# Optimization experiments

Measured on AMD Instinct MI355X. Metric: run time of the kernel, lower is better.

Reference implementation:

```python
import jax, jax.numpy as jnp
import numpy as np

D = 128

def _intra(nei, h, h_ref, att):
    # att: [2D] split into ref part and neighbor part; leakyrelu(cat(h_ref, nei_emb) @ att)
    a_ref, a_nei = att[:D], att[D:]
    nei_emb = h[nei]                                   # [N, S, D] gather
    s = h_ref @ a_ref                                  # [N]
    s = s[:, None] + nei_emb @ a_nei                   # [N, S]
    w = jax.nn.softmax(jax.nn.leaky_relu(s), axis=1)   # [N, S]
    return jnp.einsum('ns,nsd->nd', w, nei_emb)        # [N, D]

def _inter(embeds, fcW, fcb, att_inter):
    sps = jnp.stack([jnp.tanh(e @ fcW.T + fcb).mean(axis=0) for e in embeds])  # [T, D]
    beta = jax.nn.softmax(sps @ att_inter)             # [T]
    return sum(b * e for b, e in zip(beta, embeds))

def setup_inputs() -> dict:
    key = jax.random.key(0)
    ks = jax.random.split(key, 10)
    N, M, S1, S2 = 50000, 50000, 20, 10
    return {
        'h_ref': jax.random.normal(ks[0], (N, D), jnp.float32),
        'h1': jax.random.normal(ks[1], (M, D), jnp.float32),
        'h2': jax.random.normal(ks[2], (M, D), jnp.float32),
        'nei1': jax.random.randint(ks[3], (N, S1), 0, M),
        'nei2': jax.random.randint(ks[4], (N, S2), 0, M),
        'att1': jax.random.normal(ks[5], (2 * D,), jnp.float32) * 0.1,
        'att2': jax.random.normal(ks[6], (2 * D,), jnp.float32) * 0.1,
        'fcW': jax.random.normal(ks[7], (D, D), jnp.float32) * 0.1,
        'fcb': jnp.zeros((D,), jnp.float32),
        'att_inter': jax.random.normal(ks[8], (D,), jnp.float32) * 0.1,
    }

def reference(h_ref, h1, h2, nei1, nei2, att1, att2, fcW, fcb, att_inter):
    e1 = jax.nn.elu(_intra(nei1, h1, h_ref, att1))
    e2 = jax.nn.elu(_intra(nei2, h2, h_ref, att2))
    return _inter([e1, e2], fcW, fcb, att_inter)
```

## Files before the change

### kernel.cpp

```cpp
#include <hip/hip_runtime.h>
#include <hip/hip_bf16.h>
#include <math.h>

#define D 128
#define NB2 392
#define NWAVES (NB2 * 4)

typedef __attribute__((ext_vector_type(8))) short bf16x8;
typedef __attribute__((ext_vector_type(4))) float f32x4;

__device__ __forceinline__ float wave_sum(float v) {
#pragma unroll
  for (int off = 32; off; off >>= 1) v += __shfl_xor(v, off, 64);
  return v;
}

__device__ __forceinline__ unsigned bfr(float f) {
  const unsigned u = __float_as_uint(f);
  return (u + 0x7FFFu + ((u >> 16) & 1u)) >> 16;
}

__device__ __forceinline__ float fast_tanh(float x) {
  const float ez = __expf(2.f * x);
  return 1.f - 2.f / (ez + 1.f);
}

__global__ __launch_bounds__(256) void k_proj(
    const float* __restrict__ h_ref, const float* __restrict__ h1,
    const float* __restrict__ h2,
    const float* __restrict__ att1, const float* __restrict__ att2,
    float* __restrict__ q1, float* __restrict__ q2,
    float* __restrict__ p1, float* __restrict__ p2,
    unsigned* __restrict__ hb1u, unsigned* __restrict__ hb2u, int N, int M)
{
  const int lane = threadIdx.x & 63;
  const int r = blockIdx.x * 4 + (threadIdx.x >> 6);
  const int total = N + 2 * M;
  if (r >= total) return;
  if (r < N) {
    const float2 v  = *(const float2*)(h_ref + (size_t)r * D + 2 * lane);
    const float2 a1 = *(const float2*)(att1 + 2 * lane);
    const float2 a2 = *(const float2*)(att2 + 2 * lane);
    const float s1 = wave_sum(v.x * a1.x + v.y * a1.y);
    const float s2 = wave_sum(v.x * a2.x + v.y * a2.y);
    if (lane == 0) { q1[r] = s1; q2[r] = s2; }
  } else if (r < N + M) {
    const int m = r - N;
    const float2 v = *(const float2*)(h1 + (size_t)m * D + 2 * lane);
    const float2 a = *(const float2*)(att1 + D + 2 * lane);
    hb1u[(size_t)m * (D / 2) + lane] = (bfr(v.y) << 16) | bfr(v.x);
    const float s = wave_sum(v.x * a.x + v.y * a.y);
    if (lane == 0) p1[m] = s;
  } else {
    const int m = r - N - M;
    const float2 v = *(const float2*)(h2 + (size_t)m * D + 2 * lane);
    const float2 a = *(const float2*)(att2 + D + 2 * lane);
    hb2u[(size_t)m * (D / 2) + lane] = (bfr(v.y) << 16) | bfr(v.x);
    const float s = wave_sum(v.x * a.x + v.y * a.y);
    if (lane == 0) p2[m] = s;
  }
}

template<int S>
__global__ __launch_bounds__(256) void k_intra3(
    const float* __restrict__ q, const float* __restrict__ p,
    const unsigned* __restrict__ hbu, const int* __restrict__ nei,
    unsigned* __restrict__ eb, int N)
{
  const int lane = threadIdx.x & 63;
  const int n = blockIdx.x * 4 + (threadIdx.x >> 6);
  if (n >= N) return;

  const int myidx = (lane < S) ? nei[(size_t)n * S + lane] : 0;
  const float pv = (lane < S) ? p[myidx] : 0.f;
  float x = q[n] + pv;
  x = x > 0.f ? x : 0.01f * x;
  if (lane >= S) x = -1e30f;
  float m = x;
#pragma unroll
  for (int off = 32; off; off >>= 1) m = fmaxf(m, __shfl_xor(m, off, 64));
  const float ex = (lane < S) ? __expf(x - m) : 0.f;
  float sum = ex;
#pragma unroll
  for (int off = 32; off; off >>= 1) sum += __shfl_xor(sum, off, 64);
  const float w = ex / sum;

  unsigned uu[S];
#pragma unroll
  for (int s = 0; s < S; ++s) {
    const int row = __shfl(myidx, s, 64);
    uu[s] = hbu[(size_t)row * (D / 2) + lane];
  }
  float ax0 = 0.f, ay0 = 0.f, ax1 = 0.f, ay1 = 0.f;
#pragma unroll
  for (int s = 0; s < S; s += 2) {
    const float w0 = __shfl(w, s, 64);
    const float w1 = __shfl(w, s + 1, 64);
    ax0 = fmaf(w0, __uint_as_float(uu[s] << 16), ax0);
    ay0 = fmaf(w0, __uint_as_float(uu[s] & 0xFFFF0000u), ay0);
    ax1 = fmaf(w1, __uint_as_float(uu[s + 1] << 16), ax1);
    ay1 = fmaf(w1, __uint_as_float(uu[s + 1] & 0xFFFF0000u), ay1);
  }
  float ex2 = ax0 + ax1, ey2 = ay0 + ay1;
  ex2 = ex2 > 0.f ? ex2 : expm1f(ex2);
  ey2 = ey2 > 0.f ? ey2 : expm1f(ey2);
  eb[(size_t)n * (D / 2) + lane] = (bfr(ey2) << 16) | bfr(ex2);
}

__global__ __launch_bounds__(256) void k_intra3_gen(
    const float* __restrict__ q, const float* __restrict__ p,
    const unsigned* __restrict__ hbu, const int* __restrict__ nei,
    unsigned* __restrict__ eb, int N, int S)
{
  const int lane = threadIdx.x & 63;
  const int n = blockIdx.x * 4 + (threadIdx.x >> 6);
  if (n >= N) return;
  const int myidx = (lane < S) ? nei[(size_t)n * S + lane] : 0;
  const float pv = (lane < S) ? p[myidx] : 0.f;
  float x = q[n] + pv;
  x = x > 0.f ? x : 0.01f * x;
  if (lane >= S) x = -1e30f;
  float m = x;
#pragma unroll
  for (int off = 32; off; off >>= 1) m = fmaxf(m, __shfl_xor(m, off, 64));
  const float ex = (lane < S) ? __expf(x - m) : 0.f;
  float sum = ex;
#pragma unroll
  for (int off = 32; off; off >>= 1) sum += __shfl_xor(sum, off, 64);
  const float w = ex / sum;
  float ax = 0.f, ay = 0.f;
  for (int s = 0; s < S; ++s) {
    const int row = __shfl(myidx, s, 64);
    const float ws = __shfl(w, s, 64);
    const unsigned u = hbu[(size_t)row * (D / 2) + lane];
    ax = fmaf(ws, __uint_as_float(u << 16), ax);
    ay = fmaf(ws, __uint_as_float(u & 0xFFFF0000u), ay);
  }
  ax = ax > 0.f ? ax : expm1f(ax);
  ay = ay > 0.f ? ay : expm1f(ay);
  eb[(size_t)n * (D / 2) + lane] = (bfr(ay) << 16) | bfr(ax);
}

__global__ __launch_bounds__(256) void k_prep(
    const float* __restrict__ w, unsigned short* __restrict__ wb, int n)
{
  const int i = blockIdx.x * 256 + threadIdx.x;
  if (i < n) wb[i] = (unsigned short)bfr(w[i]);
}

__global__ __launch_bounds__(256) void k_fc5(
    const unsigned short* __restrict__ eb1, const unsigned short* __restrict__ eb2,
    const unsigned short* __restrict__ wb, const float* __restrict__ fcb,
    float* __restrict__ part, int N)
{
  const int path = blockIdx.y;
  const unsigned short* __restrict__ eb = path ? eb2 : eb1;
  const int lane = threadIdx.x & 63;
  const int wid  = threadIdx.x >> 6;
  const int wave = blockIdx.x * 4 + wid;
  const int r  = lane & 15;
  const int hi = lane >> 4;

  bf16x8 B[8][4];
#pragma unroll
  for (int jt = 0; jt < 8; ++jt)
#pragma unroll
    for (int kc = 0; kc < 4; ++kc)
      B[jt][kc] = *(const bf16x8*)(wb + (size_t)(jt * 16 + r) * D + kc * 32 + hi * 8);

  float bias[8];
#pragma unroll
  for (int jt = 0; jt < 8; ++jt) bias[jt] = fcb[jt * 16 + r];

  float wsum[8];
#pragma unroll
  for (int jt = 0; jt < 8; ++jt) wsum[jt] = 0.f;

  const int nstrips = (N + 15) / 16;
  for (int st = wave; st < nstrips; st += NWAVES) {
    const int n0 = st * 16;
    int na = n0 + r;
    if (na >= N) na = N - 1;
    const unsigned short* arow = eb + (size_t)na * D + hi * 8;
    bf16x8 A[4];
#pragma unroll
    for (int kc = 0; kc < 4; ++kc) A[kc] = *(const bf16x8*)(arow + kc * 32);

    f32x4 acc[8];
#pragma unroll
    for (int jt = 0; jt < 8; ++jt) acc[jt] = (f32x4){0.f, 0.f, 0.f, 0.f};
#pragma unroll
    for (int kc = 0; kc < 4; ++kc)
#pragma unroll
      for (int jt = 0; jt < 8; ++jt)
        acc[jt] = __builtin_amdgcn_mfma_f32_16x16x32_bf16(A[kc], B[jt][kc], acc[jt], 0, 0, 0);

#pragma unroll
    for (int jt = 0; jt < 8; ++jt) {
      float s = 0.f;
#pragma unroll
      for (int q = 0; q < 4; ++q) {
        const int node = n0 + hi * 4 + q;
        const float t = fast_tanh(acc[jt][q] + bias[jt]);
        s += (node < N) ? t : 0.f;
      }
      s += __shfl_xor(s, 16, 64);
      s += __shfl_xor(s, 32, 64);
      wsum[jt] += s;
    }
  }

  __shared__ float sd[4][D];
  if (lane < 16) {
#pragma unroll
    for (int jt = 0; jt < 8; ++jt) sd[wid][jt * 16 + lane] = wsum[jt];
  }
  __syncthreads();
  const int t = threadIdx.x;
  if (t < D) {
    const float v = sd[0][t] + sd[1][t] + sd[2][t] + sd[3][t];
    part[((size_t)path * NB2 + blockIdx.x) * D + t] = v;
  }
}

__global__ __launch_bounds__(256) void k_finish(
    const float* __restrict__ part, const float* __restrict__ att_inter,
    float* __restrict__ beta, float invN)
{
  const int t    = threadIdx.x;
  const int path = t >> 7;
  const int j    = t & 127;
  const int lane = t & 63;
  const int wid  = t >> 6;

  const float* __restrict__ p = part + (size_t)path * NB2 * D + j;
  float s = 0.f;
#pragma unroll 8
  for (int b = 0; b < NB2; ++b) s += p[(size_t)b * D];

  float v = (s * invN) * att_inter[j];
  v = wave_sum(v);

  __shared__ float red[4];
  if (lane == 0) red[wid] = v;
  __syncthreads();
  if (t == 0) {
    const float v0 = red[0] + red[1];
    const float v1 = red[2] + red[3];
    const float m = fmaxf(v0, v1);
    const float p0 = __expf(v0 - m), p1 = __expf(v1 - m);
    const float inv = 1.f / (p0 + p1);
    beta[0] = p0 * inv;
    beta[1] = p1 * inv;
  }
}

__global__ __launch_bounds__(256) void k_combine(
    const uint2* __restrict__ eb1v, const uint2* __restrict__ eb2v,
    const float* __restrict__ beta, float* __restrict__ outp, int total4)
{
  const float b0 = beta[0], b1 = beta[1];
  float4* out = (float4*)outp;
  int i = blockIdx.x * 256 + threadIdx.x;
  const int stride = gridDim.x * 256;
  for (; i < total4; i += stride) {
    const uint2 a = eb1v[i], b = eb2v[i];
    float4 o;
    o.x = b0 * __uint_as_float(a.x << 16)         + b1 * __uint_as_float(b.x << 16);
    o.y = b0 * __uint_as_float(a.x & 0xFFFF0000u) + b1 * __uint_as_float(b.x & 0xFFFF0000u);
    o.z = b0 * __uint_as_float(a.y << 16)         + b1 * __uint_as_float(b.y << 16);
    o.w = b0 * __uint_as_float(a.y & 0xFFFF0000u) + b1 * __uint_as_float(b.y & 0xFFFF0000u);
    out[i] = o;
  }
}

extern "C" void kernel_launch(void* const* d_in, const int* in_sizes, int n_in,
                              void* d_out, int out_size, void* d_ws, size_t ws_size,
                              hipStream_t stream) {
  const float* h_ref     = (const float*)d_in[0];
  const float* h1        = (const float*)d_in[1];
  const float* h2        = (const float*)d_in[2];
  const int*   nei1      = (const int*)d_in[3];
  const int*   nei2      = (const int*)d_in[4];
  const float* att1      = (const float*)d_in[5];
  const float* att2      = (const float*)d_in[6];
  const float* fcW       = (const float*)d_in[7];
  const float* fcb       = (const float*)d_in[8];
  const float* att_inter = (const float*)d_in[9];

  const int N  = in_sizes[0] / D;
  const int M  = in_sizes[1] / D;
  const int S1 = in_sizes[3] / N;
  const int S2 = in_sizes[4] / N;
  const size_t MX = (size_t)(M > N ? M : N) * D;

  unsigned short* bufX = (unsigned short*)d_ws;
  unsigned short* hb2  = bufX + MX;
  unsigned short* eb1  = hb2 + (size_t)M * D;
  unsigned short* wb   = eb1 + (size_t)N * D;
  float* part = (float*)(wb + D * D);
  float* beta = part + (size_t)2 * NB2 * D;
  float* q1   = beta + 2;
  float* q2   = q1 + N;
  float* p1   = q2 + N;
  float* p2   = p1 + M;
  float* out  = (float*)d_out;

  unsigned* hb1u = (unsigned*)bufX;
  unsigned* hb2u = (unsigned*)hb2;
  unsigned* eb1u = (unsigned*)eb1;
  unsigned* eb2u = (unsigned*)bufX;

  k_prep<<<(D * D + 255) / 256, 256, 0, stream>>>(fcW, wb, D * D);

  const int rows = N + 2 * M;
  k_proj<<<(rows + 3) / 4, 256, 0, stream>>>(h_ref, h1, h2, att1, att2,
                                             q1, q2, p1, p2, hb1u, hb2u, N, M);

  const dim3 gA((N + 3) / 4);
  if (S1 == 20)      k_intra3<20><<<gA, 256, 0, stream>>>(q1, p1, hb1u, nei1, eb1u, N);
  else if (S1 == 10) k_intra3<10><<<gA, 256, 0, stream>>>(q1, p1, hb1u, nei1, eb1u, N);
  else               k_intra3_gen<<<gA, 256, 0, stream>>>(q1, p1, hb1u, nei1, eb1u, N, S1);

  if (S2 == 10)      k_intra3<10><<<gA, 256, 0, stream>>>(q2, p2, hb2u, nei2, eb2u, N);
  else if (S2 == 20) k_intra3<20><<<gA, 256, 0, stream>>>(q2, p2, hb2u, nei2, eb2u, N);
  else               k_intra3_gen<<<gA, 256, 0, stream>>>(q2, p2, hb2u, nei2, eb2u, N, S2);

  const dim3 gB(NB2, 2);
  k_fc5<<<gB, 256, 0, stream>>>(eb1, (unsigned short*)bufX, wb, fcb, part, N);

  k_finish<<<1, 256, 0, stream>>>(part, att_inter, beta, 1.0f / (float)N);

  const int total4 = N * D / 4;
  int gD = (total4 + 255) / 256;
  if (gD > 2048) gD = 2048;
  k_combine<<<gD, 256, 0, stream>>>((const uint2*)eb1, (const uint2*)bufX, beta, out, total4);
}
```

Measured before the change: 134.5 us.

## Fuse fcW prep into projection and merge both intra-attention paths into one launch

Converting fcW to bf16 now happens inside the projection kernel through 64 extra wave rows, which removes a separate launch. The two intra-metapath attention kernels become a single 2D-grid launch, so both paths' gathers can run concurrently and fill the device better. To make that safe, the workspace stops aliasing hb1 and eb2 into one buffer, which costs more workspace memory. The final reduction kernel now uses 1024 threads, splitting the partial-sum scan into four chunks to shorten its serial loop.

```diff
diff --git a/kernel.cpp b/kernel.cpp
--- a/kernel.cpp
+++ b/kernel.cpp
@@ -29,13 +29,14 @@
     const float* __restrict__ h_ref, const float* __restrict__ h1,
     const float* __restrict__ h2,
     const float* __restrict__ att1, const float* __restrict__ att2,
+    const float* __restrict__ fcW, unsigned short* __restrict__ wb,
     float* __restrict__ q1, float* __restrict__ q2,
     float* __restrict__ p1, float* __restrict__ p2,
     unsigned* __restrict__ hb1u, unsigned* __restrict__ hb2u, int N, int M)
 {
   const int lane = threadIdx.x & 63;
   const int r = blockIdx.x * 4 + (threadIdx.x >> 6);
-  const int total = N + 2 * M;
+  const int total = N + 2 * M + 64;
   if (r >= total) return;
   if (r < N) {
     const float2 v  = *(const float2*)(h_ref + (size_t)r * D + 2 * lane);
@@ -51,26 +52,29 @@
     hb1u[(size_t)m * (D / 2) + lane] = (bfr(v.y) << 16) | bfr(v.x);
     const float s = wave_sum(v.x * a.x + v.y * a.y);
     if (lane == 0) p1[m] = s;
-  } else {
+  } else if (r < N + 2 * M) {
     const int m = r - N - M;
     const float2 v = *(const float2*)(h2 + (size_t)m * D + 2 * lane);
     const float2 a = *(const float2*)(att2 + D + 2 * lane);
     hb2u[(size_t)m * (D / 2) + lane] = (bfr(v.y) << 16) | bfr(v.x);
     const float s = wave_sum(v.x * a.x + v.y * a.y);
     if (lane == 0) p2[m] = s;
+  } else {
+    const int base = (r - (N + 2 * M)) * 256 + lane * 4;
+    const float4 v = *(const float4*)(fcW + base);
+    ushort4 o;
+    o.x = (unsigned short)bfr(v.x); o.y = (unsigned short)bfr(v.y);
+    o.z = (unsigned short)bfr(v.z); o.w = (unsigned short)bfr(v.w);
+    *(ushort4*)(wb + base) = o;
   }
 }
 
 template<int S>
-__global__ __launch_bounds__(256) void k_intra3(
+__device__ __forceinline__ void intra_body(
     const float* __restrict__ q, const float* __restrict__ p,
     const unsigned* __restrict__ hbu, const int* __restrict__ nei,
-    unsigned* __restrict__ eb, int N)
-{
-  const int lane = threadIdx.x & 63;
-  const int n = blockIdx.x * 4 + (threadIdx.x >> 6);
-  if (n >= N) return;
-
+    unsigned* __restrict__ eb, int N, int n, int lane)
+{
   const int myidx = (lane < S) ? nei[(size_t)n * S + lane] : 0;
   const float pv = (lane < S) ? p[myidx] : 0.f;
   float x = q[n] + pv;
@@ -105,6 +109,22 @@
   ex2 = ex2 > 0.f ? ex2 : expm1f(ex2);
   ey2 = ey2 > 0.f ? ey2 : expm1f(ey2);
   eb[(size_t)n * (D / 2) + lane] = (bfr(ey2) << 16) | bfr(ex2);
+}
+
+template<int SA, int SB>
+__global__ __launch_bounds__(256) void k_intra_dual(
+    const float* __restrict__ q1, const float* __restrict__ p1,
+    const unsigned* __restrict__ hb1, const int* __restrict__ nei1,
+    unsigned* __restrict__ eb1,
+    const float* __restrict__ q2, const float* __restrict__ p2,
+    const unsigned* __restrict__ hb2, const int* __restrict__ nei2,
+    unsigned* __restrict__ eb2, int N)
+{
+  const int lane = threadIdx.x & 63;
+  const int n = blockIdx.x * 4 + (threadIdx.x >> 6);
+  if (n >= N) return;
+  if (blockIdx.y == 0) intra_body<SA>(q1, p1, hb1, nei1, eb1, N, n, lane);
+  else                 intra_body<SB>(q2, p2, hb2, nei2, eb2, N, n, lane);
 }
 
 __global__ __launch_bounds__(256) void k_intra3_gen(
@@ -141,13 +161,6 @@
   eb[(size_t)n * (D / 2) + lane] = (bfr(ay) << 16) | bfr(ax);
 }
 
-__global__ __launch_bounds__(256) void k_prep(
-    const float* __restrict__ w, unsigned short* __restrict__ wb, int n)
-{
-  const int i = blockIdx.x * 256 + threadIdx.x;
-  if (i < n) wb[i] = (unsigned short)bfr(w[i]);
-}
-
 __global__ __launch_bounds__(256) void k_fc5(
     const unsigned short* __restrict__ eb1, const unsigned short* __restrict__ eb2,
     const unsigned short* __restrict__ wb, const float* __restrict__ fcb,
@@ -223,35 +236,43 @@
   }
 }
 
-__global__ __launch_bounds__(256) void k_finish(
+__global__ __launch_bounds__(1024) void k_finish(
     const float* __restrict__ part, const float* __restrict__ att_inter,
     float* __restrict__ beta, float invN)
 {
-  const int t    = threadIdx.x;
-  const int path = t >> 7;
-  const int j    = t & 127;
-  const int lane = t & 63;
-  const int wid  = t >> 6;
-
-  const float* __restrict__ p = part + (size_t)path * NB2 * D + j;
+  const int t     = threadIdx.x;
+  const int j     = t & 127;
+  const int path  = (t >> 7) & 1;
+  const int chunk = t >> 8;
+  const int rows  = NB2 / 4;
+
+  const float* __restrict__ p =
+      part + (size_t)path * NB2 * D + (size_t)chunk * rows * D + j;
   float s = 0.f;
-#pragma unroll 8
-  for (int b = 0; b < NB2; ++b) s += p[(size_t)b * D];
-
-  float v = (s * invN) * att_inter[j];
-  v = wave_sum(v);
-
-  __shared__ float red[4];
-  if (lane == 0) red[wid] = v;
+#pragma unroll 7
+  for (int b = 0; b < rows; ++b) s += p[(size_t)b * D];
+
+  __shared__ float sd[4][2][D];
+  sd[chunk][path][j] = s;
   __syncthreads();
-  if (t == 0) {
-    const float v0 = red[0] + red[1];
-    const float v1 = red[2] + red[3];
-    const float m = fmaxf(v0, v1);
-    const float p0 = __expf(v0 - m), p1 = __expf(v1 - m);
-    const float inv = 1.f / (p0 + p1);
-    beta[0] = p0 * inv;
-    beta[1] = p1 * inv;
+
+  if (t < 256) {
+    const float tot = sd[0][path][j] + sd[1][path][j] + sd[2][path][j] + sd[3][path][j];
+    float v = (tot * invN) * att_inter[j];
+    v = wave_sum(v);
+    __shared__ float red[4];
+    const int wid = t >> 6;
+    if ((t & 63) == 0) red[wid] = v;
+    __syncthreads();
+    if (t == 0) {
+      const float v0 = red[0] + red[1];
+      const float v1 = red[2] + red[3];
+      const float m = fmaxf(v0, v1);
+      const float p0 = __expf(v0 - m), p1 = __expf(v1 - m);
+      const float inv = 1.f / (p0 + p1);
+      beta[0] = p0 * inv;
+      beta[1] = p1 * inv;
+    }
   }
 }
 
@@ -292,12 +313,12 @@
   const int M  = in_sizes[1] / D;
   const int S1 = in_sizes[3] / N;
   const int S2 = in_sizes[4] / N;
-  const size_t MX = (size_t)(M > N ? M : N) * D;
-
-  unsigned short* bufX = (unsigned short*)d_ws;
-  unsigned short* hb2  = bufX + MX;
-  unsigned short* eb1  = hb2 + (size_t)M * D;
-  unsigned short* wb   = eb1 + (size_t)N * D;
+
+  unsigned short* hb1 = (unsigned short*)d_ws;
+  unsigned short* hb2 = hb1 + (size_t)M * D;
+  unsigned short* eb1 = hb2 + (size_t)M * D;
+  unsigned short* eb2 = eb1 + (size_t)N * D;
+  unsigned short* wb  = eb2 + (size_t)N * D;
   float* part = (float*)(wb + D * D);
   float* beta = part + (size_t)2 * NB2 * D;
   float* q1   = beta + 2;
@@ -306,33 +327,41 @@
   float* p2   = p1 + M;
   float* out  = (float*)d_out;
 
-  unsigned* hb1u = (unsigned*)bufX;
+  unsigned* hb1u = (unsigned*)hb1;
   unsigned* hb2u = (unsigned*)hb2;
   unsigned* eb1u = (unsigned*)eb1;
-  unsigned* eb2u = (unsigned*)bufX;
-
-  k_prep<<<(D * D + 255) / 256, 256, 0, stream>>>(fcW, wb, D * D);
-
-  const int rows = N + 2 * M;
-  k_proj<<<(rows + 3) / 4, 256, 0, stream>>>(h_ref, h1, h2, att1, att2,
+  unsigned* eb2u = (unsigned*)eb2;
+
+  const int rows = N + 2 * M + 64;
+  k_proj<<<(rows + 3) / 4, 256, 0, stream>>>(h_ref, h1, h2, att1, att2, fcW, wb,
                                              q1, q2, p1, p2, hb1u, hb2u, N, M);
 
-  const dim3 gA((N + 3) / 4);
-  if (S1 == 20)      k_intra3<20><<<gA, 256, 0, stream>>>(q1, p1, hb1u, nei1, eb1u, N);
-  else if (S1 == 10) k_intra3<10><<<gA, 256, 0, stream>>>(q1, p1, hb1u, nei1, eb1u, N);
-  else               k_intra3_gen<<<gA, 256, 0, stream>>>(q1, p1, hb1u, nei1, eb1u, N, S1);
-
-  if (S2 == 10)      k_intra3<10><<<gA, 256, 0, stream>>>(q2, p2, hb2u, nei2, eb2u, N);
-  else if (S2 == 20) k_intra3<20><<<gA, 256, 0, stream>>>(q2, p2, hb2u, nei2, eb2u, N);
-  else               k_intra3_gen<<<gA, 256, 0, stream>>>(q2, p2, hb2u, nei2, eb2u, N, S2);
+  const dim3 gA((N + 3) / 4, 2);
+  if (S1 == 20 && S2 == 10)
+    k_intra_dual<20, 10><<<gA, 256, 0, stream>>>(q1, p1, hb1u, nei1, eb1u,
+                                                 q2, p2, hb2u, nei2, eb2u, N);
+  else if (S1 == 10 && S2 == 20)
+    k_intra_dual<10, 20><<<gA, 256, 0, stream>>>(q1, p1, hb1u, nei1, eb1u,
+                                                 q2, p2, hb2u, nei2, eb2u, N);
+  else if (S1 == 10 && S2 == 10)
+    k_intra_dual<10, 10><<<gA, 256, 0, stream>>>(q1, p1, hb1u, nei1, eb1u,
+                                                 q2, p2, hb2u, nei2, eb2u, N);
+  else if (S1 == 20 && S2 == 20)
+    k_intra_dual<20, 20><<<gA, 256, 0, stream>>>(q1, p1, hb1u, nei1, eb1u,
+                                                 q2, p2, hb2u, nei2, eb2u, N);
+  else {
+    const dim3 g1((N + 3) / 4);
+    k_intra3_gen<<<g1, 256, 0, stream>>>(q1, p1, hb1u, nei1, eb1u, N, S1);
+    k_intra3_gen<<<g1, 256, 0, stream>>>(q2, p2, hb2u, nei2, eb2u, N, S2);
+  }
 
   const dim3 gB(NB2, 2);
-  k_fc5<<<gB, 256, 0, stream>>>(eb1, (unsigned short*)bufX, wb, fcb, part, N);
-
-  k_finish<<<1, 256, 0, stream>>>(part, att_inter, beta, 1.0f / (float)N);
+  k_fc5<<<gB, 256, 0, stream>>>(eb1, eb2, wb, fcb, part, N);
+
+  k_finish<<<1, 1024, 0, stream>>>(part, att_inter, beta, 1.0f / (float)N);
 
   const int total4 = N * D / 4;
   int gD = (total4 + 255) / 256;
   if (gD > 2048) gD = 2048;
-  k_combine<<<gD, 256, 0, stream>>>((const uint2*)eb1, (const uint2*)bufX, beta, out, total4);
-}
+  k_combine<<<gD, 256, 0, stream>>>((const uint2*)eb1, (const uint2*)eb2, beta, out, total4);
+}
```

After: 119.3 us. 1.13x faster.
